# Kernel optimization log

Measured on AMD Instinct MI355X. Metric: run time of the kernel, lower is better.

## Reference

```python
import jax, jax.numpy as jnp
import numpy as np

D_MODEL = 1024
NUM_HEADS = 16

def _dense_params(key, d_in, d_out):
    kw, _ = jax.random.split(key)
    # flax default: lecun_normal kernel, zeros bias
    W = jax.random.normal(kw, (d_in, d_out), dtype=jnp.float32) / np.sqrt(d_in)
    b = jnp.zeros((d_out,), dtype=jnp.float32)
    return W, b

def setup_inputs() -> dict:
    key = jax.random.key(0)
    ks = jax.random.split(key, 8)
    B, Tx, Tc = 2, 2048, 2048
    x = jax.random.normal(ks[0], (B, Tx, D_MODEL), dtype=jnp.float32)
    context = jax.random.normal(ks[1], (B, Tc, D_MODEL), dtype=jnp.float32)
    Wq, bq = _dense_params(ks[2], D_MODEL, D_MODEL)
    Wks, bks = _dense_params(ks[3], D_MODEL, D_MODEL)
    Wvs, bvs = _dense_params(ks[4], D_MODEL, D_MODEL)
    Wkc, bkc = _dense_params(ks[5], D_MODEL, D_MODEL)
    Wvc, bvc = _dense_params(ks[6], D_MODEL, D_MODEL)
    Wo, bo = _dense_params(ks[7], D_MODEL, D_MODEL)
    return {"x": x, "context": context,
            "Wq": Wq, "bq": bq, "Wks": Wks, "bks": bks, "Wvs": Wvs, "bvs": bvs,
            "Wkc": Wkc, "bkc": bkc, "Wvc": Wvc, "bvc": bvc, "Wo": Wo, "bo": bo}

def _split_heads(t, H):
    B, T, C = t.shape
    return t.reshape(B, T, H, C // H).transpose(0, 2, 1, 3)  # [B,H,T,hd]

def reference(x, context, Wq, bq, Wks, bks, Wvs, bvs, Wkc, bkc, Wvc, bvc, Wo, bo):
    H = NUM_HEADS
    head_dim = D_MODEL // H
    q = x @ Wq + bq
    k = jnp.concatenate([x @ Wks + bks, context @ Wkc + bkc], axis=1)
    v = jnp.concatenate([x @ Wvs + bvs, context @ Wvc + bvc], axis=1)
    q = _split_heads(q, H)  # [B,H,Tq,hd]
    k = _split_heads(k, H)  # [B,H,Tk,hd]
    v = _split_heads(v, H)
    attn = jnp.einsum('bhqd,bhkd->bhqk', q, k) / jnp.sqrt(jnp.float32(head_dim))
    attn = jax.nn.softmax(attn, axis=-1)
    out = jnp.einsum('bhqk,bhkd->bhqd', attn, v)
    B, _, Tq, _ = out.shape
    out = out.transpose(0, 2, 1, 3).reshape(B, Tq, D_MODEL)
    return out @ Wo + bo
```

## Files before the change

### kernel.cpp

```cpp
#include <hip/hip_runtime.h>
#include <hip/hip_bf16.h>
#include <math.h>


typedef _Float16 f16;
typedef _Float16 f16x8 __attribute__((ext_vector_type(8)));
typedef _Float16 f16x4v __attribute__((ext_vector_type(4)));
typedef float    f32x4 __attribute__((ext_vector_type(4)));

#define MFMA_F16(a, b, c) __builtin_amdgcn_mfma_f32_16x16x32_f16((a), (b), (c), 0, 0, 0)

#define QSCALE 0.18033688011112042f

__device__ __forceinline__ void glds16(const f16* g, f16* l) {
    __builtin_amdgcn_global_load_lds(
        (const __attribute__((address_space(1))) void*)g,
        (__attribute__((address_space(3))) void*)l, 16, 0, 0);
}

__global__ __launch_bounds__(256) void prep(
    const float4* __restrict__ x, const float4* __restrict__ ctx,
    f16x4v* __restrict__ xb, f16x4v* __restrict__ cb,
    const float* __restrict__ W0, const float* __restrict__ W1,
    const float* __restrict__ W2, const float* __restrict__ W3,
    const float* __restrict__ W4, const float* __restrict__ W5,
    f16* __restrict__ wt)
{
    if (blockIdx.x < 8192) {
        const int n4 = (2 * 2048 * 1024) / 4;
        int i = blockIdx.x * 256 + threadIdx.x;
        float4 v;
        f16x4v* dst;
        if (i < n4) { v = x[i];        dst = xb + i; }
        else        { v = ctx[i - n4]; dst = cb + (i - n4); }
        f16x4v h = { (f16)v.x, (f16)v.y, (f16)v.z, (f16)v.w };
        *dst = h;
        return;
    }
    const int idx = blockIdx.x - 8192;
    const int z = idx >> 10, rem = idx & 1023;
    const float* Ws[6] = { W0, W1, W2, W3, W4, W5 };
    const float* W = Ws[z];
    f16* Wt = wt + (size_t)z * (1024 * 1024);

    __shared__ float tile[32][33];
    const int tx = threadIdx.x & 31, ty = threadIdx.x >> 5;
    const int n0 = (rem & 31) * 32, k0 = (rem >> 5) * 32;

#pragma unroll
    for (int i = 0; i < 4; ++i) {
        int r = i * 8 + ty;
        tile[r][tx] = W[(size_t)(k0 + r) * 1024 + n0 + tx];
    }
    __syncthreads();
#pragma unroll
    for (int i = 0; i < 4; ++i) {
        int r = i * 8 + ty;
        Wt[(size_t)(n0 + r) * 1024 + k0 + tx] = (f16)tile[tx][r];
    }
}

#define GEMM_PROLOGUE(BN)                                                     \
    const int m0 = blockIdx.x * 128, n0 = blockIdx.y * (BN);                  \
    const int tid = threadIdx.x;                                              \
    const int w = tid >> 6, lane = tid & 63, quad = lane >> 4, l15 = lane & 15;\
    const int wm = (w >> 1) * 64, wn = (w & 1) * ((BN) / 2);                  \
    const int qsw = (quad ^ ((l15 >> 1) & 3)) * 8;                            \
    int gA[2], gB[(BN) / 64];                                                 \
    _Pragma("unroll")                                                         \
    for (int p = 0; p < 2; ++p) {                                             \
        int s = tid + p * 256;                                                \
        int r = (s >> 2) & 127, c = (s & 3) ^ ((s >> 3) & 3);                 \
        gA[p] = (m0 + r) * 1024 + c * 8;                                      \
    }                                                                         \
    _Pragma("unroll")                                                         \
    for (int p = 0; p < (BN) / 64; ++p) {                                     \
        int s = tid + p * 256;                                                \
        int r = (s >> 2) & ((BN) - 1), c = (s & 3) ^ ((s >> 3) & 3);          \
        gB[p] = (n0 + r) * 1024 + c * 8;                                      \
    }

#define GEMM_STAGE_TO(BN, buf, koff)                                          \
    _Pragma("unroll")                                                         \
    for (int p = 0; p < 2; ++p)                                               \
        glds16(&A[gA[p] + (koff)], &As[buf][(p * 256 + w * 64) * 8]);         \
    _Pragma("unroll")                                                         \
    for (int p = 0; p < (BN) / 64; ++p)                                       \
        glds16(&Bt[gB[p] + (koff)], &Bs[buf][(p * 256 + w * 64) * 8]);

__global__ __launch_bounds__(256) void proj_gemm(
    const f16* __restrict__ xb, const f16* __restrict__ cb,
    const f16* __restrict__ wt,
    const float* __restrict__ bq, const float* __restrict__ bks,
    const float* __restrict__ bkc, const float* __restrict__ bvs,
    const float* __restrict__ bvc,
    f16* __restrict__ qbuf, f16* __restrict__ kbuf, f16* __restrict__ vbuf)
{
    __shared__ alignas(16) f16 As[2][128 * 32];
    __shared__ alignas(16) f16 Bs[2][128 * 32];

    const int z = blockIdx.z;
    const f16* A = (z == 0 || z == 1 || z == 3) ? xb : cb;
    const int wslot = (z == 0) ? 0 : (z == 1) ? 1 : (z == 2) ? 3 : (z == 3) ? 2 : 4;
    const f16* Bt = wt + (size_t)wslot * 1048576;
    const float* bias = (z == 0) ? bq : (z == 1) ? bks : (z == 2) ? bkc
                        : (z == 3) ? bvs : bvc;
    const int roff = (z == 2 || z == 4) ? 2048 : 0;

    GEMM_PROLOGUE(128)
    f32x4 acc[4][4] = {};

    GEMM_STAGE_TO(128, 0, 0)

    for (int k0 = 0; k0 < 1024; k0 += 32) {
        const int cur = (k0 >> 5) & 1;
        __syncthreads();
        if (k0 + 32 < 1024) {
            GEMM_STAGE_TO(128, cur ^ 1, k0 + 32)
        }
        f16x8 a[4], b[4];
#pragma unroll
        for (int i = 0; i < 4; ++i)
            a[i] = *(const f16x8*)&As[cur][(wm + i * 16 + l15) * 32 + qsw];
#pragma unroll
        for (int i = 0; i < 4; ++i)
            b[i] = *(const f16x8*)&Bs[cur][(wn + i * 16 + l15) * 32 + qsw];
#pragma unroll
        for (int mi = 0; mi < 4; ++mi)
#pragma unroll
            for (int ni = 0; ni < 4; ++ni)
                acc[mi][ni] = MFMA_F16(a[mi], b[ni], acc[mi][ni]);
    }

#pragma unroll
    for (int mi = 0; mi < 4; ++mi) {
#pragma unroll
        for (int r = 0; r < 4; ++r) {
            int row = m0 + wm + mi * 16 + quad * 4 + r;
            int b_ = row >> 11, tok = row & 2047;
#pragma unroll
            for (int ni = 0; ni < 4; ++ni) {
                int col = n0 + wn + ni * 16 + l15;
                float v = acc[mi][ni][r] + bias[col];
                int bh = b_ * 16 + (col >> 6);
                int tg = roff + tok;
                if (z == 0) {
                    qbuf[((size_t)bh * 2048 + tok) * 64 + (col & 63)] = (f16)(v * QSCALE);
                } else if (z <= 2) {
                    kbuf[(size_t)bh * 262144 + (size_t)(tg >> 6) * 4096
                         + (size_t)((col >> 5) & 1) * 2048 + (tg & 63) * 32 + (col & 31)] = (f16)v;
                } else {
                    vbuf[(size_t)bh * 262144 + (size_t)tg * 64 + (col & 63)] = (f16)v;
                }
            }
        }
    }
}

__global__ __launch_bounds__(256) void transpose_v(
    const f16* __restrict__ vbuf, f16* __restrict__ vt)
{
    const int t = threadIdx.x;
    const int mt = t >> 3, md = t & 7;
    const int tok0 = blockIdx.x * 256 + mt * 8;
    const int z = blockIdx.y;
    f16x8 in[8];
#pragma unroll
    for (int i = 0; i < 8; ++i)
        in[i] = *(const f16x8*)&vbuf[((size_t)z * 4096 + tok0 + i) * 64 + md * 8];
    f16x8 ov[8];
#pragma unroll
    for (int j = 0; j < 8; ++j)
#pragma unroll
        for (int i = 0; i < 8; ++i) ov[j][i] = in[i][j];
    const int kt = tok0 >> 6, kks = (tok0 >> 5) & 1, kko = tok0 & 31;
#pragma unroll
    for (int j = 0; j < 8; ++j)
        *(f16x8*)&vt[(size_t)z * 262144 + (size_t)kt * 4096 + kks * 2048
                     + (md * 8 + j) * 32 + kko] = ov[j];
}

__global__ __launch_bounds__(256, 4) void attn_kernel(
    const f16* __restrict__ q, const f16* __restrict__ kb,
    const f16* __restrict__ vtb, f16* __restrict__ osplit,
    float* __restrict__ lsplit)
{
    __shared__ alignas(16) f16 K_lds[4096];
    __shared__ alignas(16) f16 V_lds[4096];
    __shared__ alignas(16) f16 P_lds[128 * 72];

    const int tid = threadIdx.x;
    const int w = tid >> 6, lane = tid & 63, quad = lane >> 4, l15 = lane & 15;
    const int bh = blockIdx.x, qt = blockIdx.y, sp = blockIdx.z;
    const int qbase = qt * 128;

    f16x8 qa[2][2];
#pragma unroll
    for (int nq = 0; nq < 2; ++nq) {
        const size_t qaddr =
            ((size_t)bh * 2048 + qbase + w * 32 + nq * 16 + l15) * 64 + quad * 8;
        qa[nq][0] = *(const f16x8*)&q[qaddr];
        qa[nq][1] = *(const f16x8*)&q[qaddr + 32];
    }

    f16x8 ones;
#pragma unroll
    for (int j = 0; j < 8; ++j) ones[j] = (f16)1.0f;

    f32x4 o_acc[2][4] = {};
    f32x4 l_acc[2] = {};

    const f16* ktile = kb + (size_t)bh * 262144 + (size_t)sp * 131072;
    const f16* vtile = vtb + (size_t)bh * 262144 + (size_t)sp * 131072;

    const int sco = ((tid >> 2) * 4 + ((tid & 3) ^ ((tid >> 3) & 3))) * 8;
    const int qsw = (quad ^ ((l15 >> 1) & 3)) * 8;
    const int wslot = w * 512;
    const int lslot = wslot + lane * 8;

    glds16(ktile + sco,        &K_lds[wslot]);
    glds16(ktile + 2048 + sco, &K_lds[2048 + wslot]);
    glds16(vtile + sco,        &V_lds[wslot]);
    glds16(vtile + 2048 + sco, &V_lds[2048 + wslot]);

    for (int kt = 0; kt < 32; ++kt) {
        __syncthreads();

        ktile += 4096; vtile += 4096;
        f16x8 kn0, kn1, vn0, vn1;
        if (kt != 31) {
            kn0 = *(const f16x8*)&ktile[sco];
            kn1 = *(const f16x8*)&ktile[2048 + sco];
            vn0 = *(const f16x8*)&vtile[sco];
            vn1 = *(const f16x8*)&vtile[2048 + sco];
        }

#pragma unroll
        for (int mt = 0; mt < 4; ++mt) {
            f16x8 ka0 = *(const f16x8*)&K_lds[(mt * 16 + l15) * 32 + qsw];
            f16x8 ka1 = *(const f16x8*)&K_lds[2048 + (mt * 16 + l15) * 32 + qsw];
            f32x4 s[2];
            __builtin_amdgcn_s_setprio(1);
#pragma unroll
            for (int nq = 0; nq < 2; ++nq) {
                f32x4 t = {};
                t = MFMA_F16(ka0, qa[nq][0], t);
                t = MFMA_F16(ka1, qa[nq][1], t);
                s[nq] = t;
            }
            __builtin_amdgcn_s_setprio(0);
#pragma unroll
            for (int nq = 0; nq < 2; ++nq) {
                f16x4v pk;
#pragma unroll
                for (int r = 0; r < 4; ++r)
                    pk[r] = (f16)__builtin_amdgcn_exp2f(s[nq][r]);
                *(f16x4v*)&P_lds[(w * 32 + nq * 16 + l15) * 72 + mt * 16 + quad * 4] = pk;
            }
        }

        f16x8 pa[2][2];
#pragma unroll
        for (int nq = 0; nq < 2; ++nq)
#pragma unroll
            for (int ks = 0; ks < 2; ++ks)
                pa[nq][ks] = *(const f16x8*)&P_lds[(w * 32 + nq * 16 + l15) * 72 + ks * 32 + quad * 8];

        __builtin_amdgcn_s_setprio(1);
#pragma unroll
        for (int nq = 0; nq < 2; ++nq) {
            l_acc[nq] = MFMA_F16(ones, pa[nq][0], l_acc[nq]);
            l_acc[nq] = MFMA_F16(ones, pa[nq][1], l_acc[nq]);
        }

#pragma unroll
        for (int dt = 0; dt < 4; ++dt) {
            f16x8 vb0 = *(const f16x8*)&V_lds[(dt * 16 + l15) * 32 + qsw];
            f16x8 vb1 = *(const f16x8*)&V_lds[2048 + (dt * 16 + l15) * 32 + qsw];
#pragma unroll
            for (int nq = 0; nq < 2; ++nq) {
                o_acc[nq][dt] = MFMA_F16(pa[nq][0], vb0, o_acc[nq][dt]);
                o_acc[nq][dt] = MFMA_F16(pa[nq][1], vb1, o_acc[nq][dt]);
            }
        }
        __builtin_amdgcn_s_setprio(0);

        __syncthreads();
        if (kt != 31) {
            *(f16x8*)&K_lds[lslot]        = kn0;
            *(f16x8*)&K_lds[2048 + lslot] = kn1;
            *(f16x8*)&V_lds[lslot]        = vn0;
            *(f16x8*)&V_lds[2048 + lslot] = vn1;
        }
    }

    const size_t sb = (size_t)(sp * 32 + bh) * 2048 + qbase;
#pragma unroll
    for (int nq = 0; nq < 2; ++nq) {
        if (quad == 0)
            lsplit[sb + w * 32 + nq * 16 + l15] = l_acc[nq][0];
#pragma unroll
        for (int r = 0; r < 4; ++r) {
            float lr = __shfl(l_acc[nq][0], quad * 4 + r, 64);
            float inv = 1.0f / lr;
            int ql = w * 32 + nq * 16 + quad * 4 + r;
            size_t obase = (sb + ql) * 64;
#pragma unroll
            for (int dt = 0; dt < 4; ++dt)
                osplit[obase + dt * 16 + l15] = (f16)(o_acc[nq][dt][r] * inv);
        }
    }
}

__global__ __launch_bounds__(256) void combine(
    const f16* __restrict__ osplit, const float* __restrict__ lsplit,
    f16* __restrict__ abuf)
{
    int idx = blockIdx.x * 256 + threadIdx.x;
    int d8 = idx & 7;
    int row = (idx >> 3) & 2047;
    int bh = idx >> 14;
    int b = bh >> 4, h = bh & 15;
    size_t base1 = ((size_t)bh * 2048 + row) * 64 + d8 * 8;
    size_t base2 = ((size_t)(32 + bh) * 2048 + row) * 64 + d8 * 8;
    float l1 = lsplit[bh * 2048 + row];
    float l2 = lsplit[(32 + bh) * 2048 + row];
    float inv = 1.0f / (l1 + l2);
    float w1 = l1 * inv, w2 = l2 * inv;
    f16x8 a = *(const f16x8*)&osplit[base1];
    f16x8 c = *(const f16x8*)&osplit[base2];
    f16x8 out;
#pragma unroll
    for (int j = 0; j < 8; ++j)
        out[j] = (f16)(w1 * (float)a[j] + w2 * (float)c[j]);
    *(f16x8*)&abuf[((size_t)(b * 2048 + row)) * 1024 + h * 64 + d8 * 8] = out;
}

__global__ __launch_bounds__(256) void out_gemm(
    const f16* __restrict__ abuf, const f16* __restrict__ wt5,
    const float* __restrict__ bo, float* __restrict__ out)
{
    __shared__ alignas(16) f16 As[2][128 * 32];
    __shared__ alignas(16) f16 Bs[2][64 * 32];

    const f16* A = abuf;
    const f16* Bt = wt5;

    GEMM_PROLOGUE(64)
    f32x4 acc[4][2] = {};

    GEMM_STAGE_TO(64, 0, 0)

    for (int k0 = 0; k0 < 1024; k0 += 32) {
        const int cur = (k0 >> 5) & 1;
        __syncthreads();
        if (k0 + 32 < 1024) {
            GEMM_STAGE_TO(64, cur ^ 1, k0 + 32)
        }
        f16x8 a[4], b[2];
#pragma unroll
        for (int i = 0; i < 4; ++i)
            a[i] = *(const f16x8*)&As[cur][(wm + i * 16 + l15) * 32 + qsw];
#pragma unroll
        for (int i = 0; i < 2; ++i)
            b[i] = *(const f16x8*)&Bs[cur][(wn + i * 16 + l15) * 32 + qsw];
#pragma unroll
        for (int mi = 0; mi < 4; ++mi)
#pragma unroll
            for (int ni = 0; ni < 2; ++ni)
                acc[mi][ni] = MFMA_F16(a[mi], b[ni], acc[mi][ni]);
    }

#pragma unroll
    for (int mi = 0; mi < 4; ++mi) {
#pragma unroll
        for (int r = 0; r < 4; ++r) {
            int row = m0 + wm + mi * 16 + quad * 4 + r;
#pragma unroll
            for (int ni = 0; ni < 2; ++ni) {
                int col = n0 + wn + ni * 16 + l15;
                out[(size_t)row * 1024 + col] = acc[mi][ni][r] + bo[col];
            }
        }
    }
}

extern "C" void kernel_launch(void* const* d_in, const int* in_sizes, int n_in,
                              void* d_out, int out_size, void* d_ws, size_t ws_size,
                              hipStream_t stream)
{
    (void)in_sizes; (void)n_in; (void)out_size; (void)ws_size;

    const float* x    = (const float*)d_in[0];
    const float* ctx  = (const float*)d_in[1];
    const float* Wq   = (const float*)d_in[2];  const float* bq  = (const float*)d_in[3];
    const float* Wks  = (const float*)d_in[4];  const float* bks = (const float*)d_in[5];
    const float* Wvs  = (const float*)d_in[6];  const float* bvs = (const float*)d_in[7];
    const float* Wkc  = (const float*)d_in[8];  const float* bkc = (const float*)d_in[9];
    const float* Wvc  = (const float*)d_in[10]; const float* bvc = (const float*)d_in[11];
    const float* Wo   = (const float*)d_in[12]; const float* bo  = (const float*)d_in[13];

    char* ws = (char*)d_ws;
    f16*   xb     = (f16*)(ws + 0);
    f16*   cb     = (f16*)(ws + 8388608);
    f16*   vt     = (f16*)(ws + 0);
    f16*   wt     = (f16*)(ws + 16777216);
    float* lsplit = (float*)(ws + 16777216);
    f16*   qbuf   = (f16*)(ws + 29360128);
    f16*   kbuf   = (f16*)(ws + 37748736);
    f16*   vbuf   = (f16*)(ws + 54525952);
    f16*   osplit = (f16*)(ws + 54525952);
    f16*   abuf   = (f16*)(ws + 71303168);

    prep<<<14336, 256, 0, stream>>>((const float4*)x, (const float4*)ctx,
                                    (f16x4v*)xb, (f16x4v*)cb,
                                    Wq, Wks, Wvs, Wkc, Wvc, Wo, wt);

    proj_gemm<<<dim3(32, 8, 5), 256, 0, stream>>>(
        xb, cb, wt, bq, bks, bkc, bvs, bvc, qbuf, kbuf, vbuf);

    transpose_v<<<dim3(16, 32), 256, 0, stream>>>(vbuf, vt);

    attn_kernel<<<dim3(32, 16, 2), 256, 0, stream>>>(qbuf, kbuf, vt, osplit, lsplit);

    combine<<<2048, 256, 0, stream>>>(osplit, lsplit, abuf);

    out_gemm<<<dim3(32, 16), 256, 0, stream>>>(abuf, wt + 5 * 1048576, bo, (float*)d_out);
}
```

Baseline: 300.0 us.

## Switch attention to 32x32x16 MFMA and keep P in registers via permlane swap

Rewrites the attention inner loop to use 32x32x16 f16 MFMAs with S computed transposed (K as A operand), so each lane holds a full query row's scores. P fragments are built in registers with permlane32_swap instead of going through a P_lds shared-memory round trip. The row sum is taken with scalar adds rather than an extra ones-MFMA. This removes the LDS traffic and bank pressure for P and the wasted MFMAs for the denominator. The cost is a changed register layout and higher accumulator register pressure, which may affect occupancy.

```diff
diff --git a/kernel.cpp b/kernel.cpp
--- a/kernel.cpp
+++ b/kernel.cpp
@@ -6,9 +6,13 @@
 typedef _Float16 f16;
 typedef _Float16 f16x8 __attribute__((ext_vector_type(8)));
 typedef _Float16 f16x4v __attribute__((ext_vector_type(4)));
+typedef _Float16 f16x2 __attribute__((ext_vector_type(2)));
 typedef float    f32x4 __attribute__((ext_vector_type(4)));
-
-#define MFMA_F16(a, b, c) __builtin_amdgcn_mfma_f32_16x16x32_f16((a), (b), (c), 0, 0, 0)
+typedef float    f32x16 __attribute__((ext_vector_type(16)));
+typedef unsigned u32x4v __attribute__((ext_vector_type(4)));
+
+#define MFMA_F16(a, b, c)  __builtin_amdgcn_mfma_f32_16x16x32_f16((a), (b), (c), 0, 0, 0)
+#define MFMA32_F16(a, b, c) __builtin_amdgcn_mfma_f32_32x32x16_f16((a), (b), (c), 0, 0, 0)
 
 #define QSCALE 0.18033688011112042f
 
@@ -16,6 +20,11 @@
     __builtin_amdgcn_global_load_lds(
         (const __attribute__((address_space(1))) void*)g,
         (__attribute__((address_space(3))) void*)l, 16, 0, 0);
+}
+
+__device__ __forceinline__ unsigned pk16(float a, float b) {
+    f16x2 t = { (f16)a, (f16)b };
+    return __builtin_bit_cast(unsigned, t);
 }
 
 __global__ __launch_bounds__(256) void prep(
@@ -187,34 +196,29 @@
 {
     __shared__ alignas(16) f16 K_lds[4096];
     __shared__ alignas(16) f16 V_lds[4096];
-    __shared__ alignas(16) f16 P_lds[128 * 72];
 
     const int tid = threadIdx.x;
-    const int w = tid >> 6, lane = tid & 63, quad = lane >> 4, l15 = lane & 15;
+    const int w = tid >> 6, lane = tid & 63;
+    const int l31 = lane & 31, h = lane >> 5;
     const int bh = blockIdx.x, qt = blockIdx.y, sp = blockIdx.z;
     const int qbase = qt * 128;
 
-    f16x8 qa[2][2];
-#pragma unroll
-    for (int nq = 0; nq < 2; ++nq) {
-        const size_t qaddr =
-            ((size_t)bh * 2048 + qbase + w * 32 + nq * 16 + l15) * 64 + quad * 8;
-        qa[nq][0] = *(const f16x8*)&q[qaddr];
-        qa[nq][1] = *(const f16x8*)&q[qaddr + 32];
-    }
-
-    f16x8 ones;
-#pragma unroll
-    for (int j = 0; j < 8; ++j) ones[j] = (f16)1.0f;
-
-    f32x4 o_acc[2][4] = {};
-    f32x4 l_acc[2] = {};
+    f16x8 qa[4];
+    {
+        const size_t qrow = ((size_t)bh * 2048 + qbase + w * 32 + l31) * 64;
+#pragma unroll
+        for (int kc = 0; kc < 4; ++kc)
+            qa[kc] = *(const f16x8*)&q[qrow + kc * 16 + h * 8];
+    }
+
+    f32x16 o_acc[2] = {};
+    float l_part = 0.f;
 
     const f16* ktile = kb + (size_t)bh * 262144 + (size_t)sp * 131072;
     const f16* vtile = vtb + (size_t)bh * 262144 + (size_t)sp * 131072;
 
     const int sco = ((tid >> 2) * 4 + ((tid & 3) ^ ((tid >> 3) & 3))) * 8;
-    const int qsw = (quad ^ ((l15 >> 1) & 3)) * 8;
+    const int ksw = (l31 >> 1) & 3;
     const int wslot = w * 512;
     const int lslot = wslot + lane * 8;
 
@@ -236,54 +240,55 @@
         }
 
 #pragma unroll
-        for (int mt = 0; mt < 4; ++mt) {
-            f16x8 ka0 = *(const f16x8*)&K_lds[(mt * 16 + l15) * 32 + qsw];
-            f16x8 ka1 = *(const f16x8*)&K_lds[2048 + (mt * 16 + l15) * 32 + qsw];
-            f32x4 s[2];
+        for (int mt = 0; mt < 2; ++mt) {
+            f32x16 s = {};
             __builtin_amdgcn_s_setprio(1);
 #pragma unroll
-            for (int nq = 0; nq < 2; ++nq) {
-                f32x4 t = {};
-                t = MFMA_F16(ka0, qa[nq][0], t);
-                t = MFMA_F16(ka1, qa[nq][1], t);
-                s[nq] = t;
+            for (int kc = 0; kc < 4; ++kc) {
+                f16x8 ka = *(const f16x8*)&K_lds[(kc >> 1) * 2048
+                             + (mt * 32 + l31) * 32
+                             + ((((kc & 1) * 2 + h) ^ ksw)) * 8];
+                s = MFMA32_F16(ka, qa[kc], s);
             }
             __builtin_amdgcn_s_setprio(0);
-#pragma unroll
-            for (int nq = 0; nq < 2; ++nq) {
-                f16x4v pk;
-#pragma unroll
-                for (int r = 0; r < 4; ++r)
-                    pk[r] = (f16)__builtin_amdgcn_exp2f(s[nq][r]);
-                *(f16x4v*)&P_lds[(w * 32 + nq * 16 + l15) * 72 + mt * 16 + quad * 4] = pk;
+
+            float pe[16];
+#pragma unroll
+            for (int i = 0; i < 16; ++i) pe[i] = __builtin_amdgcn_exp2f(s[i]);
+
+            {
+                float t0 = (pe[0] + pe[1]) + (pe[2] + pe[3]);
+                float t1 = (pe[4] + pe[5]) + (pe[6] + pe[7]);
+                float t2 = (pe[8] + pe[9]) + (pe[10] + pe[11]);
+                float t3 = (pe[12] + pe[13]) + (pe[14] + pe[15]);
+                l_part += (t0 + t1) + (t2 + t3);
             }
-        }
-
-        f16x8 pa[2][2];
-#pragma unroll
-        for (int nq = 0; nq < 2; ++nq)
-#pragma unroll
-            for (int ks = 0; ks < 2; ++ks)
-                pa[nq][ks] = *(const f16x8*)&P_lds[(w * 32 + nq * 16 + l15) * 72 + ks * 32 + quad * 8];
-
-        __builtin_amdgcn_s_setprio(1);
-#pragma unroll
-        for (int nq = 0; nq < 2; ++nq) {
-            l_acc[nq] = MFMA_F16(ones, pa[nq][0], l_acc[nq]);
-            l_acc[nq] = MFMA_F16(ones, pa[nq][1], l_acc[nq]);
-        }
-
-#pragma unroll
-        for (int dt = 0; dt < 4; ++dt) {
-            f16x8 vb0 = *(const f16x8*)&V_lds[(dt * 16 + l15) * 32 + qsw];
-            f16x8 vb1 = *(const f16x8*)&V_lds[2048 + (dt * 16 + l15) * 32 + qsw];
-#pragma unroll
-            for (int nq = 0; nq < 2; ++nq) {
-                o_acc[nq][dt] = MFMA_F16(pa[nq][0], vb0, o_acc[nq][dt]);
-                o_acc[nq][dt] = MFMA_F16(pa[nq][1], vb1, o_acc[nq][dt]);
+
+#pragma unroll
+            for (int c = 0; c < 2; ++c) {
+                const int cb = c * 8;
+                unsigned X0 = pk16(pe[cb + 0], pe[cb + 1]);
+                unsigned X1 = pk16(pe[cb + 2], pe[cb + 3]);
+                unsigned Y0 = pk16(pe[cb + 4], pe[cb + 5]);
+                unsigned Y1 = pk16(pe[cb + 6], pe[cb + 7]);
+                auto r0 = __builtin_amdgcn_permlane32_swap(X0, Y0, false, false);
+                auto r1 = __builtin_amdgcn_permlane32_swap(X1, Y1, false, false);
+                u32x4v pw;
+                pw[0] = r0[0]; pw[1] = r1[0]; pw[2] = r0[1]; pw[3] = r1[1];
+                f16x8 pfrag = __builtin_bit_cast(f16x8, pw);
+
+                const int kchunk = mt * 2 + c;
+                __builtin_amdgcn_s_setprio(1);
+#pragma unroll
+                for (int db = 0; db < 2; ++db) {
+                    f16x8 va = *(const f16x8*)&V_lds[(kchunk >> 1) * 2048
+                                 + (db * 32 + l31) * 32
+                                 + (((((kchunk & 1) * 2 + h)) ^ ksw)) * 8];
+                    o_acc[db] = MFMA32_F16(va, pfrag, o_acc[db]);
+                }
+                __builtin_amdgcn_s_setprio(0);
             }
         }
-        __builtin_amdgcn_s_setprio(0);
 
         __syncthreads();
         if (kt != 31) {
@@ -294,20 +299,21 @@
         }
     }
 
+    float lf = l_part + __shfl_xor(l_part, 32, 64);
+    float inv = 1.0f / lf;
     const size_t sb = (size_t)(sp * 32 + bh) * 2048 + qbase;
-#pragma unroll
-    for (int nq = 0; nq < 2; ++nq) {
-        if (quad == 0)
-            lsplit[sb + w * 32 + nq * 16 + l15] = l_acc[nq][0];
-#pragma unroll
-        for (int r = 0; r < 4; ++r) {
-            float lr = __shfl(l_acc[nq][0], quad * 4 + r, 64);
-            float inv = 1.0f / lr;
-            int ql = w * 32 + nq * 16 + quad * 4 + r;
-            size_t obase = (sb + ql) * 64;
-#pragma unroll
-            for (int dt = 0; dt < 4; ++dt)
-                osplit[obase + dt * 16 + l15] = (f16)(o_acc[nq][dt][r] * inv);
+    const int row = w * 32 + l31;
+    if (h == 0) lsplit[sb + row] = lf;
+    const size_t obase = (sb + row) * 64;
+#pragma unroll
+    for (int db = 0; db < 2; ++db) {
+#pragma unroll
+        for (int g = 0; g < 4; ++g) {
+            f16x4v ov;
+#pragma unroll
+            for (int i = 0; i < 4; ++i)
+                ov[i] = (f16)(o_acc[db][g * 4 + i] * inv);
+            *(f16x4v*)&osplit[obase + db * 32 + g * 8 + h * 4] = ov;
         }
     }
 }
```

After: 297.9 us. Within noise of the previous version (-0.7%).
